# Optimization experiments

Measured on AMD Instinct MI355X. Metric: run time of the kernel, lower is better.

## Reference

```python
import jax, jax.numpy as jnp
import numpy as np

NUM_HEADS = 12


def setup_inputs() -> dict:
    key = jax.random.key(0)
    k_x, k_m, k_qkv, k_proj = jax.random.split(key, 4)
    B, N, C = 2, 2048, 768
    x = jax.random.normal(k_x, (B, N, C), dtype=jnp.float32)
    # binary key mask: 1 = attend, 0 = masked out
    mask = jax.random.randint(k_m, (B, N), 0, 2).astype(jnp.int32)
    # torch Linear(dim, dim*3, bias=False): stored here as [in, out]
    w_qkv = jax.random.normal(k_qkv, (C, 3 * C), dtype=jnp.float32) * 0.02
    w_proj = jax.random.normal(k_proj, (C, C), dtype=jnp.float32) * 0.02
    b_proj = jnp.zeros((C,), dtype=jnp.float32)
    return {"x": x, "mask": mask, "w_qkv": w_qkv, "w_proj": w_proj, "b_proj": b_proj}


def reference(x, mask, w_qkv, w_proj, b_proj):
    B, N, C = x.shape
    H = NUM_HEADS
    hd = C // H
    scale = hd ** -0.5
    qkv = (x @ w_qkv).reshape(B, N, 3, H, hd)
    q, k, v = jnp.moveaxis(qkv, 2, 0)            # each [B, N, H, hd]
    attn = jnp.einsum('bnhd,bmhd->bhnm', q, k) * scale  # [B, H, N, N]
    # faithful masked_softmax: unstable exp (no max subtraction), mask keys, renormalize
    m = mask.astype(x.dtype)[:, None, None, :]   # [B, 1, 1, N]
    x_exp = jnp.exp(attn) * m
    attn = x_exp / x_exp.sum(-1, keepdims=True)
    out = jnp.einsum('bhnm,bmhd->bnhd', attn, v).reshape(B, N, C)
    return out @ w_proj + b_proj
```

## Files before the change

kernel.cpp:

```cpp
#include <hip/hip_runtime.h>
#include <cstdint>

#define NB 2
#define NSEQ 2048
#define CDIM 768
#define NH 12
#define HD 64
#define NTOK (NB*NSEQ)
#define QKV_COLS (3*CDIM)
#define NBLK ((NSEQ/64)*NH*NB)

typedef short bf16x8 __attribute__((ext_vector_type(8)));
typedef short bf16x4 __attribute__((ext_vector_type(4)));
typedef float f32x4  __attribute__((ext_vector_type(4)));
typedef short short4v __attribute__((ext_vector_type(4)));
typedef unsigned int uint4v __attribute__((ext_vector_type(4)));

#define MFMA16(a,b,c) __builtin_amdgcn_mfma_f32_16x16x32_bf16(a,b,c,0,0,0)

__device__ __forceinline__ short f2b(float f) {
    uint32_t u = __builtin_bit_cast(uint32_t, f);
    u += 0x7fffu + ((u >> 16) & 1u);
    return (short)(u >> 16);
}
__device__ __forceinline__ float b2f(short s) {
    return __builtin_bit_cast(float, (uint32_t)((uint32_t)(unsigned short)s << 16));
}
__device__ __forceinline__ unsigned pack2(float a, float b) {
    unsigned ua = __builtin_bit_cast(unsigned, a) + 0x7fffu;
    unsigned ub = __builtin_bit_cast(unsigned, b) + 0x7fffu;
    return __builtin_amdgcn_perm(ub, ua, 0x07060302u);
}
__device__ __forceinline__ float fexp2(float x) {
#if __has_builtin(__builtin_amdgcn_exp2f)
    return __builtin_amdgcn_exp2f(x);
#else
    return __expf(x * 0.69314718055994531f);
#endif
}
__device__ __forceinline__ void gll16(const short* g, short* l) {
    __builtin_amdgcn_global_load_lds(
        (const __attribute__((address_space(1))) unsigned int*)g,
        (__attribute__((address_space(3))) unsigned int*)l, 16, 0, 0);
}

__global__ __launch_bounds__(256) void prep_kernel(
    const float* __restrict__ x, const float* __restrict__ w_qkv,
    const float* __restrict__ w_proj, const int* __restrict__ mask,
    short* __restrict__ xb, short* __restrict__ wqt, short* __restrict__ wpt,
    short* __restrict__ maskb)
{
    __shared__ float tile[32][33];
    const int bid = blockIdx.x, t = threadIdx.x;
    if (bid < 3072) {
        int i = bid * 256 + t;
        float4 v = ((const float4*)x)[i];
        short4v o = { f2b(v.x), f2b(v.y), f2b(v.z), f2b(v.w) };
        ((short4v*)xb)[i] = o;
        return;
    }
    if (bid >= 5376) {
        int i = ((bid - 5376) << 11) + (t << 3);
        int4 a = *(const int4*)(mask + i);
        int4 c = *(const int4*)(mask + i + 4);
        const short NEG = (short)0xC680;
        short4v o0 = { a.x ? (short)0 : NEG, a.y ? (short)0 : NEG,
                       a.z ? (short)0 : NEG, a.w ? (short)0 : NEG };
        short4v o1 = { c.x ? (short)0 : NEG, c.y ? (short)0 : NEG,
                       c.z ? (short)0 : NEG, c.w ? (short)0 : NEG };
        *(short4v*)(maskb + i) = o0;
        *(short4v*)(maskb + i + 4) = o1;
        return;
    }
    const float* w; short* wt; int K, NC, n0, k0;
    if (bid < 3072 + 1728) {
        int r = bid - 3072;
        w = w_qkv; wt = wqt; K = CDIM; NC = QKV_COLS;
        n0 = (r % 72) * 32; k0 = (r / 72) * 32;
    } else {
        int r = bid - 4800;
        w = w_proj; wt = wpt; K = CDIM; NC = CDIM;
        n0 = (r % 24) * 32; k0 = (r / 24) * 32;
    }
    #pragma unroll
    for (int i = 0; i < 4; ++i) {
        int idx = t + i * 256; int r = idx >> 5, c = idx & 31;
        tile[r][c] = w[(size_t)(k0 + r) * NC + n0 + c];
    }
    __syncthreads();
    #pragma unroll
    for (int i = 0; i < 4; ++i) {
        int idx = t + i * 256; int r = idx >> 5, c = idx & 31;
        wt[(size_t)(n0 + r) * K + k0 + c] = f2b(tile[c][r]);
    }
}

__global__ __launch_bounds__(256) void gemm_qkv(
    const short* __restrict__ A ,
    const short* __restrict__ B ,
    short* __restrict__ qb, short* __restrict__ kb, short* __restrict__ vt)
{
    __shared__ short As[128 * 32];
    __shared__ short Bs[128 * 32];
    const int t = threadIdx.x;
    const int lane = t & 63, wid = t >> 6;
    const int quad = lane >> 4, l16 = lane & 15;
    const int wA = wid >> 1, wB = wid & 1;
    const int n0 = blockIdx.x * 128;
    const int m0 = blockIdx.y * 128;

    const int srow = wid * 16 + (lane >> 2), schunk = (lane & 3) * 8;
    const short* ag0 = A + (size_t)(n0 + srow) * CDIM + schunk;
    const short* ag1 = ag0 + (size_t)64 * CDIM;
    const short* bg0 = B + (size_t)(m0 + srow) * CDIM + schunk;
    const short* bg1 = bg0 + (size_t)64 * CDIM;
    short* asl0 = &As[(wid * 16) * 32];
    short* asl1 = &As[(wid * 16 + 64) * 32];
    short* bsl0 = &Bs[(wid * 16) * 32];
    short* bsl1 = &Bs[(wid * 16 + 64) * 32];

    f32x4 acc[4][4] = {};
    for (int k0 = 0; k0 < CDIM; k0 += 32) {
        __syncthreads();
        gll16(ag0 + k0, asl0);
        gll16(ag1 + k0, asl1);
        gll16(bg0 + k0, bsl0);
        gll16(bg1 + k0, bsl1);
        __syncthreads();
        bf16x8 af[4], bf[4];
        #pragma unroll
        for (int i = 0; i < 4; ++i)
            af[i] = *(const bf16x8*)&As[(wA*64 + i*16 + l16) * 32 + quad*8];
        #pragma unroll
        for (int j = 0; j < 4; ++j)
            bf[j] = *(const bf16x8*)&Bs[(wB*64 + j*16 + l16) * 32 + quad*8];
        #pragma unroll
        for (int i = 0; i < 4; ++i)
            #pragma unroll
            for (int j = 0; j < 4; ++j)
                acc[i][j] = MFMA16(af[i], bf[j], acc[i][j]);
    }

    const int colbase = n0 + wA * 64;
    const int s = colbase / CDIM;
    const int h = (colbase - s * CDIM) >> 6;
    const int b = m0 >> 11;
    const size_t bh = (size_t)(b * NH + h);
    const float qsc = (s == 0) ? 0.18033688011112042f : 1.0f;
    #pragma unroll
    for (int i = 0; i < 4; ++i) {
        const int d0 = i*16 + quad*4;
        #pragma unroll
        for (int j = 0; j < 4; ++j) {
            int tok = (m0 + wB*64 + j*16 + l16) & (NSEQ - 1);
            if (s < 2) {
                short* dst = (s == 0 ? qb : kb) + (bh * NSEQ + tok) * HD + d0;
                short4v o = { f2b(acc[i][j][0] * qsc), f2b(acc[i][j][1] * qsc),
                              f2b(acc[i][j][2] * qsc), f2b(acc[i][j][3] * qsc) };
                *(short4v*)dst = o;
            } else {
                short* dst = vt + (bh * HD + d0) * NSEQ + tok;
                #pragma unroll
                for (int r = 0; r < 4; ++r)
                    dst[(size_t)r * NSEQ] = f2b(acc[i][j][r]);
            }
        }
    }
}

#define STAGE_K(KT, BUF) do {                                                    \
    short* kb_ = (BUF);                                                          \
    _Pragma("unroll")                                                            \
    for (int j = 0; j < 4; ++j)                                                  \
        gll16(kp + (size_t)((KT) + rK[j]) * HD + cK[j]*8,                        \
              kb_ + wid*2048 + j*512);                                           \
} while (0)

#define STAGE_V(KT) do {                                                         \
    _Pragma("unroll")                                                            \
    for (int j = 0; j < 4; ++j)                                                  \
        gll16(vp + (size_t)dV[j] * NSEQ + (KT) + cV[j]*8,                        \
              Vb + wid*2048 + j*512);                                            \
} while (0)

#define QKBODY(KT, KBUF) do {                                                    \
    const short* KsB_ = (KBUF);                                                  \
    _Pragma("unroll")                                                            \
    for (int ks = 0; ks < 4; ++ks) {                                             \
        short4v mi0_ = *(const short4v*)&Msk[(KT) + ks*16 + qrow4];              \
        short4v mi1_ = *(const short4v*)&Msk[(KT) + 64 + ks*16 + qrow4];         \
        const int kro_ = (ks*16 + l16) * 64;                                     \
        bf16x8 kf00_ = *(const bf16x8*)&KsB_[kro_ + kc0];                        \
        bf16x8 kf01_ = *(const bf16x8*)&KsB_[kro_ + kc1];                        \
        bf16x8 kf10_ = *(const bf16x8*)&KsB_[4096 + kro_ + kc0];                 \
        bf16x8 kf11_ = *(const bf16x8*)&KsB_[4096 + kro_ + kc1];                 \
        f32x4 s0_ = { b2f(mi0_[0]), b2f(mi0_[1]),                                \
                      b2f(mi0_[2]), b2f(mi0_[3]) };                              \
        f32x4 s1_ = { b2f(mi1_[0]), b2f(mi1_[1]),                                \
                      b2f(mi1_[2]), b2f(mi1_[3]) };                              \
        s0_ = MFMA16(kf00_, qf0, s0_);                                           \
        s0_ = MFMA16(kf01_, qf1, s0_);                                           \
        s1_ = MFMA16(kf10_, qf0, s1_);                                           \
        s1_ = MFMA16(kf11_, qf1, s1_);                                           \
        float e0 = fexp2(s0_[0]);                                                \
        float e1 = fexp2(s0_[1]);                                                \
        float e2 = fexp2(s0_[2]);                                                \
        float e3 = fexp2(s0_[3]);                                                \
        float f0 = fexp2(s1_[0]);                                                \
        float f1 = fexp2(s1_[1]);                                                \
        float f2 = fexp2(s1_[2]);                                                \
        float f3 = fexp2(s1_[3]);                                                \
        uint4v pk_ = { pack2(e0, e1), pack2(e2, e3),                             \
                       pack2(f0, f1), pack2(f2, f3) };                           \
        pb[ks] = __builtin_bit_cast(bf16x8, pk_);                                \
    }                                                                            \
} while (0)

#define PVBODY() do {                                                            \
    _Pragma("unroll")                                                            \
    for (int ks = 0; ks < 4; ++ks)                                               \
        lacc = MFMA16(onesv, pb[ks], lacc);                                      \
    _Pragma("unroll")                                                            \
    for (int it = 0; it < 4; ++it) {                                             \
        const int vrow_ = (it*16 + l16) * 128;                                   \
        _Pragma("unroll")                                                        \
        for (int ks = 0; ks < 4; ++ks) {                                         \
            const int gl_ = (((ks*2 + qh) ^ l16) << 3) + vsub;                   \
            const int gh_ = (((8 + ks*2 + qh) ^ l16) << 3) + vsub;               \
            bf16x4 lo_ = *(const bf16x4*)&Vb[vrow_ + gl_];                       \
            bf16x4 hi_ = *(const bf16x4*)&Vb[vrow_ + gh_];                       \
            bf16x8 vf_ = __builtin_shufflevector(lo_, hi_, 0,1,2,3,4,5,6,7);     \
            o_acc[it] = MFMA16(vf_, pb[ks], o_acc[it]);                          \
        }                                                                        \
    }                                                                            \
} while (0)

__global__ __launch_bounds__(256, 3) void attn_kernel(
    const short* __restrict__ qb, const short* __restrict__ kb,
    const short* __restrict__ vt, const short* __restrict__ maskb,
    short* __restrict__ ao)
{
    __shared__ __align__(16) short Kb[2][8192];
    __shared__ __align__(16) short Vb[8192];
    __shared__ __align__(16) short Msk[2048];

    const int t = threadIdx.x;
    const int lane = t & 63, wid = t >> 6;
    const int quad = lane >> 4, l16 = lane & 15;
    const int id = blockIdx.x;
    const int idx = id >> 3;
    const int bh = (id & 7) + ((idx % 3) << 3);
    const int q0 = (idx / 3) << 6;
    const int b = bh / NH, h = bh - b * NH;
    const size_t hoff = (size_t)bh * NSEQ * HD;
    const short* qp = qb + hoff;
    const short* kp = kb + hoff;
    const short* vp = vt + hoff;
    const int qrow4 = quad * 4;

    int rK[4], cK[4], dV[4], cV[4];
    #pragma unroll
    for (int j = 0; j < 4; ++j) {
        int o = wid * 4096 + j * 1024 + lane * 16;
        rK[j] = o >> 7;
        cK[j] = ((o >> 4) & 7) ^ (rK[j] & 7);
        dV[j] = o >> 8;
        cV[j] = ((o >> 4) & 15) ^ (dV[j] & 15);
    }
    const int r7 = l16 & 7;
    const int kc0 = ((quad     ^ r7) << 3);
    const int kc1 = (((quad+4) ^ r7) << 3);
    const int qh = quad >> 1;
    const int vsub = (quad & 1) * 4;

    bf16x8 qf0, qf1;
    {
        const short* qr = qp + (size_t)(q0 + wid*16 + l16) * HD + quad*8;
        qf0 = *(const bf16x8*)qr;
        qf1 = *(const bf16x8*)(qr + 32);
    }

    const short one_ = (short)0x3F80;
    const bf16x8 onesv = { one_, one_, one_, one_, one_, one_, one_, one_ };

    f32x4 o_acc[4] = {};
    f32x4 lacc = {};
    bf16x8 pb[4];

    STAGE_K(0, Kb[0]);
    gll16(maskb + b * NSEQ + t * 8, Msk + wid * 512);
    __syncthreads();

    for (int kt = 0; kt < NSEQ; kt += 256) {
        STAGE_V(kt);
        STAGE_K(kt + 128, Kb[1]);
        QKBODY(kt, Kb[0]);
        __syncthreads();
        PVBODY();
        __syncthreads();

        STAGE_V(kt + 128);
        STAGE_K((kt + 256) & (NSEQ - 1), Kb[0]);
        QKBODY(kt + 128, Kb[1]);
        __syncthreads();
        PVBODY();
        __syncthreads();
    }

    const float inv = 1.0f / lacc[0];

    const int tok = b * NSEQ + q0 + wid*16 + l16;
    short* dst = ao + (size_t)tok * CDIM + h * HD + qrow4;
    #pragma unroll
    for (int it = 0; it < 4; ++it) {
        short4v o = { f2b(o_acc[it][0] * inv), f2b(o_acc[it][1] * inv),
                      f2b(o_acc[it][2] * inv), f2b(o_acc[it][3] * inv) };
        *(short4v*)(dst + it*16) = o;
    }
}

__global__ __launch_bounds__(256) void gemm_proj(
    const short* __restrict__ A ,
    const short* __restrict__ B ,
    const float* __restrict__ bias, float* __restrict__ out)
{
    __shared__ short As[128 * 32];
    __shared__ short Bs[128 * 32];
    const int t = threadIdx.x;
    const int lane = t & 63, wid = t >> 6;
    const int quad = lane >> 4, l16 = lane & 15;
    const int wA = wid >> 1, wB = wid & 1;
    const int n0 = blockIdx.x * 128;
    const int m0 = blockIdx.y * 128;

    const int srow = wid * 16 + (lane >> 2), schunk = (lane & 3) * 8;
    const short* ag0 = A + (size_t)(n0 + srow) * CDIM + schunk;
    const short* ag1 = ag0 + (size_t)64 * CDIM;
    const short* bg0 = B + (size_t)(m0 + srow) * CDIM + schunk;
    const short* bg1 = bg0 + (size_t)64 * CDIM;
    short* asl0 = &As[(wid * 16) * 32];
    short* asl1 = &As[(wid * 16 + 64) * 32];
    short* bsl0 = &Bs[(wid * 16) * 32];
    short* bsl1 = &Bs[(wid * 16 + 64) * 32];

    f32x4 acc[4][4] = {};
    for (int k0 = 0; k0 < CDIM; k0 += 32) {
        __syncthreads();
        gll16(ag0 + k0, asl0);
        gll16(ag1 + k0, asl1);
        gll16(bg0 + k0, bsl0);
        gll16(bg1 + k0, bsl1);
        __syncthreads();
        bf16x8 af[4], bf[4];
        #pragma unroll
        for (int i = 0; i < 4; ++i)
            af[i] = *(const bf16x8*)&As[(wA*64 + i*16 + l16) * 32 + quad*8];
        #pragma unroll
        for (int j = 0; j < 4; ++j)
            bf[j] = *(const bf16x8*)&Bs[(wB*64 + j*16 + l16) * 32 + quad*8];
        #pragma unroll
        for (int i = 0; i < 4; ++i)
            #pragma unroll
            for (int j = 0; j < 4; ++j)
                acc[i][j] = MFMA16(af[i], bf[j], acc[i][j]);
    }

    #pragma unroll
    for (int i = 0; i < 4; ++i) {
        int col0 = n0 + wA*64 + i*16 + quad*4;
        float4 bias4 = *(const float4*)&bias[col0];
        #pragma unroll
        for (int j = 0; j < 4; ++j) {
            int tok = m0 + wB*64 + j*16 + l16;
            float4 o = { acc[i][j][0] + bias4.x, acc[i][j][1] + bias4.y,
                         acc[i][j][2] + bias4.z, acc[i][j][3] + bias4.w };
            *(float4*)(out + (size_t)tok * CDIM + col0) = o;
        }
    }
}

extern "C" void kernel_launch(void* const* d_in, const int* in_sizes, int n_in,
                              void* d_out, int out_size, void* d_ws, size_t ws_size,
                              hipStream_t stream)
{
    const float* x      = (const float*)d_in[0];
    const int*   mask   = (const int*)d_in[1];
    const float* w_qkv  = (const float*)d_in[2];
    const float* w_proj = (const float*)d_in[3];
    const float* b_proj = (const float*)d_in[4];
    float* out = (float*)d_out;

    const size_t SZ = (size_t)NTOK * CDIM;
    short* xb  = (short*)d_ws;
    short* wqt = xb  + SZ;
    short* wpt = wqt + (size_t)QKV_COLS * CDIM;
    short* qb  = wpt + (size_t)CDIM * CDIM;
    short* kb  = qb  + SZ;
    short* vt  = kb  + SZ;
    short* ao  = vt  + SZ;
    short* maskb = ao + SZ;

    dim3 blk(256);
    prep_kernel<<<dim3(5378), blk, 0, stream>>>(x, w_qkv, w_proj, mask,
                                                xb, wqt, wpt, maskb);
    gemm_qkv<<<dim3(QKV_COLS/128, NTOK/128), blk, 0, stream>>>(wqt, xb, qb, kb, vt);
    attn_kernel<<<dim3(NBLK), blk, 0, stream>>>(qb, kb, vt, maskb, ao);
    gemm_proj<<<dim3(CDIM/128, NTOK/128), blk, 0, stream>>>(wpt, ao, b_proj, out);
}
```

Before: 167.6 us.

## Split attention warps into query and key groups with LDS partial-sum reduction

Each wave now handles 32 query rows over half of each 128-key tile, instead of 16 query rows over the whole tile. Every K and V fragment read from LDS is therefore reused across two query sub-tiles, roughly halving LDS fragment reads per MFMA. The two key-group partial outputs and row sums are combined at the end through shared memory. The trade-offs are doubled accumulator registers, which may hurt occupancy at 3 blocks per CU, and an extra reduction and barrier. The last K prefetch is also skipped instead of wrapping around.

```diff
diff --git a/kernel.cpp b/kernel.cpp
--- a/kernel.cpp
+++ b/kernel.cpp
@@ -184,53 +184,60 @@
 } while (0)
 
 #define QKBODY(KT, KBUF) do {                                                    \
-    const short* KsB_ = (KBUF);                                                  \
+    const short* KsB_ = (KBUF) + kg*4096;                                        \
     _Pragma("unroll")                                                            \
-    for (int ks = 0; ks < 4; ++ks) {                                             \
-        short4v mi0_ = *(const short4v*)&Msk[(KT) + ks*16 + qrow4];              \
-        short4v mi1_ = *(const short4v*)&Msk[(KT) + 64 + ks*16 + qrow4];         \
+    for (int ks = 0; ks < 2; ++ks) {                                             \
+        short4v mi0_ = *(const short4v*)&Msk[(KT) + kg*64 + ks*16 + qrow4];      \
+        short4v mi1_ = *(const short4v*)&Msk[(KT) + kg*64 + 32 + ks*16 + qrow4]; \
         const int kro_ = (ks*16 + l16) * 64;                                     \
         bf16x8 kf00_ = *(const bf16x8*)&KsB_[kro_ + kc0];                        \
         bf16x8 kf01_ = *(const bf16x8*)&KsB_[kro_ + kc1];                        \
-        bf16x8 kf10_ = *(const bf16x8*)&KsB_[4096 + kro_ + kc0];                 \
-        bf16x8 kf11_ = *(const bf16x8*)&KsB_[4096 + kro_ + kc1];                 \
-        f32x4 s0_ = { b2f(mi0_[0]), b2f(mi0_[1]),                                \
-                      b2f(mi0_[2]), b2f(mi0_[3]) };                              \
-        f32x4 s1_ = { b2f(mi1_[0]), b2f(mi1_[1]),                                \
-                      b2f(mi1_[2]), b2f(mi1_[3]) };                              \
-        s0_ = MFMA16(kf00_, qf0, s0_);                                           \
-        s0_ = MFMA16(kf01_, qf1, s0_);                                           \
-        s1_ = MFMA16(kf10_, qf0, s1_);                                           \
-        s1_ = MFMA16(kf11_, qf1, s1_);                                           \
-        float e0 = fexp2(s0_[0]);                                                \
-        float e1 = fexp2(s0_[1]);                                                \
-        float e2 = fexp2(s0_[2]);                                                \
-        float e3 = fexp2(s0_[3]);                                                \
-        float f0 = fexp2(s1_[0]);                                                \
-        float f1 = fexp2(s1_[1]);                                                \
-        float f2 = fexp2(s1_[2]);                                                \
-        float f3 = fexp2(s1_[3]);                                                \
-        uint4v pk_ = { pack2(e0, e1), pack2(e2, e3),                             \
-                       pack2(f0, f1), pack2(f2, f3) };                           \
-        pb[ks] = __builtin_bit_cast(bf16x8, pk_);                                \
+        bf16x8 kf10_ = *(const bf16x8*)&KsB_[2048 + kro_ + kc0];                 \
+        bf16x8 kf11_ = *(const bf16x8*)&KsB_[2048 + kro_ + kc1];                 \
+        f32x4 m0v_ = { b2f(mi0_[0]), b2f(mi0_[1]),                               \
+                       b2f(mi0_[2]), b2f(mi0_[3]) };                             \
+        f32x4 m1v_ = { b2f(mi1_[0]), b2f(mi1_[1]),                               \
+                       b2f(mi1_[2]), b2f(mi1_[3]) };                             \
+        _Pragma("unroll")                                                        \
+        for (int jq = 0; jq < 2; ++jq) {                                         \
+            f32x4 s0_ = m0v_, s1_ = m1v_;                                        \
+            s0_ = MFMA16(kf00_, qf[jq][0], s0_);                                 \
+            s0_ = MFMA16(kf01_, qf[jq][1], s0_);                                 \
+            s1_ = MFMA16(kf10_, qf[jq][0], s1_);                                 \
+            s1_ = MFMA16(kf11_, qf[jq][1], s1_);                                 \
+            float e0 = fexp2(s0_[0]);                                            \
+            float e1 = fexp2(s0_[1]);                                            \
+            float e2 = fexp2(s0_[2]);                                            \
+            float e3 = fexp2(s0_[3]);                                            \
+            float f0 = fexp2(s1_[0]);                                            \
+            float f1 = fexp2(s1_[1]);                                            \
+            float f2 = fexp2(s1_[2]);                                            \
+            float f3 = fexp2(s1_[3]);                                            \
+            uint4v pk_ = { pack2(e0, e1), pack2(e2, e3),                         \
+                           pack2(f0, f1), pack2(f2, f3) };                       \
+            pb[jq][ks] = __builtin_bit_cast(bf16x8, pk_);                        \
+        }                                                                        \
     }                                                                            \
 } while (0)
 
 #define PVBODY() do {                                                            \
     _Pragma("unroll")                                                            \
-    for (int ks = 0; ks < 4; ++ks)                                               \
-        lacc = MFMA16(onesv, pb[ks], lacc);                                      \
+    for (int ks = 0; ks < 2; ++ks) {                                             \
+        lacc[0] = MFMA16(onesv, pb[0][ks], lacc[0]);                             \
+        lacc[1] = MFMA16(onesv, pb[1][ks], lacc[1]);                             \
+    }                                                                            \
     _Pragma("unroll")                                                            \
     for (int it = 0; it < 4; ++it) {                                             \
         const int vrow_ = (it*16 + l16) * 128;                                   \
         _Pragma("unroll")                                                        \
-        for (int ks = 0; ks < 4; ++ks) {                                         \
-            const int gl_ = (((ks*2 + qh) ^ l16) << 3) + vsub;                   \
-            const int gh_ = (((8 + ks*2 + qh) ^ l16) << 3) + vsub;               \
+        for (int ks = 0; ks < 2; ++ks) {                                         \
+            const int gl_ = (((kg*8 + ks*2 + qh) ^ l16) << 3) + vsub;            \
+            const int gh_ = (((kg*8 + 4 + ks*2 + qh) ^ l16) << 3) + vsub;        \
             bf16x4 lo_ = *(const bf16x4*)&Vb[vrow_ + gl_];                       \
             bf16x4 hi_ = *(const bf16x4*)&Vb[vrow_ + gh_];                       \
             bf16x8 vf_ = __builtin_shufflevector(lo_, hi_, 0,1,2,3,4,5,6,7);     \
-            o_acc[it] = MFMA16(vf_, pb[ks], o_acc[it]);                          \
+            o_acc[0][it] = MFMA16(vf_, pb[0][ks], o_acc[0][it]);                 \
+            o_acc[1][it] = MFMA16(vf_, pb[1][ks], o_acc[1][it]);                 \
         }                                                                        \
     }                                                                            \
 } while (0)
@@ -247,6 +254,7 @@
     const int t = threadIdx.x;
     const int lane = t & 63, wid = t >> 6;
     const int quad = lane >> 4, l16 = lane & 15;
+    const int qg = wid >> 1, kg = wid & 1;
     const int id = blockIdx.x;
     const int idx = id >> 3;
     const int bh = (id & 7) + ((idx % 3) << 3);
@@ -273,19 +281,21 @@
     const int qh = quad >> 1;
     const int vsub = (quad & 1) * 4;
 
-    bf16x8 qf0, qf1;
+    bf16x8 qf[2][2];
     {
-        const short* qr = qp + (size_t)(q0 + wid*16 + l16) * HD + quad*8;
-        qf0 = *(const bf16x8*)qr;
-        qf1 = *(const bf16x8*)(qr + 32);
+        const short* qr = qp + (size_t)(q0 + qg*32 + l16) * HD + quad*8;
+        qf[0][0] = *(const bf16x8*)qr;
+        qf[0][1] = *(const bf16x8*)(qr + 32);
+        qf[1][0] = *(const bf16x8*)(qr + 16*HD);
+        qf[1][1] = *(const bf16x8*)(qr + 16*HD + 32);
     }
 
     const short one_ = (short)0x3F80;
     const bf16x8 onesv = { one_, one_, one_, one_, one_, one_, one_, one_ };
 
-    f32x4 o_acc[4] = {};
-    f32x4 lacc = {};
-    bf16x8 pb[4];
+    f32x4 o_acc[2][4] = {};
+    f32x4 lacc[2] = {};
+    bf16x8 pb[2][2];
 
     STAGE_K(0, Kb[0]);
     gll16(maskb + b * NSEQ + t * 8, Msk + wid * 512);
@@ -300,22 +310,45 @@
         __syncthreads();
 
         STAGE_V(kt + 128);
-        STAGE_K((kt + 256) & (NSEQ - 1), Kb[0]);
+        if (kt + 256 < NSEQ) STAGE_K(kt + 256, Kb[0]);
         QKBODY(kt + 128, Kb[1]);
         __syncthreads();
         PVBODY();
         __syncthreads();
     }
 
-    const float inv = 1.0f / lacc[0];
-
-    const int tok = b * NSEQ + q0 + wid*16 + l16;
-    short* dst = ao + (size_t)tok * CDIM + h * HD + qrow4;
-    #pragma unroll
-    for (int it = 0; it < 4; ++it) {
-        short4v o = { f2b(o_acc[it][0] * inv), f2b(o_acc[it][1] * inv),
-                      f2b(o_acc[it][2] * inv), f2b(o_acc[it][3] * inv) };
-        *(short4v*)(dst + it*16) = o;
+    f32x4* red = (f32x4*)Kb;
+    const int rbase = (qg*64 + lane) * 9;
+    if (kg == 1) {
+        #pragma unroll
+        for (int jq = 0; jq < 2; ++jq)
+            #pragma unroll
+            for (int it = 0; it < 4; ++it)
+                red[rbase + jq*4 + it] = o_acc[jq][it];
+        f32x4 lv = { lacc[0][0], lacc[1][0], 0.f, 0.f };
+        red[rbase + 8] = lv;
+    }
+    __syncthreads();
+    if (kg == 0) {
+        f32x4 lv = red[rbase + 8];
+        const float inv0 = 1.0f / (lacc[0][0] + lv[0]);
+        const float inv1 = 1.0f / (lacc[1][0] + lv[1]);
+        #pragma unroll
+        for (int jq = 0; jq < 2; ++jq) {
+            const float inv = jq ? inv1 : inv0;
+            const int tok = b * NSEQ + q0 + qg*32 + jq*16 + l16;
+            short* dst = ao + (size_t)tok * CDIM + h * HD + qrow4;
+            #pragma unroll
+            for (int it = 0; it < 4; ++it) {
+                f32x4 o_ = o_acc[jq][it];
+                f32x4 r_ = red[rbase + jq*4 + it];
+                short4v o = { f2b((o_[0] + r_[0]) * inv),
+                              f2b((o_[1] + r_[1]) * inv),
+                              f2b((o_[2] + r_[2]) * inv),
+                              f2b((o_[3] + r_[3]) * inv) };
+                *(short4v*)(dst + it*16) = o;
+            }
+        }
     }
 }
 
```

New measurement: 159.7 us. -4.7%, faster.
